# Kernel tuning notes

Measured on AMD Instinct MI355X. Metric: run time of the kernel, lower is better.

Reference implementation:

```python
import jax, jax.numpy as jnp
import numpy as np

EPS = 1e-5  # PyG LayerNorm default eps
N, E, D, H, B = 100000, 1600000, 128, 256, 64


def _gcn_edge_weights(src, dst, n):
    # GCNConv symmetric normalization with added self-loops:
    # deg[i] = in-degree(i) + 1 ; w(j->i) = deg[j]^-1/2 * deg[i]^-1/2
    deg = jax.ops.segment_sum(jnp.ones(src.shape[0], jnp.float32), dst, num_segments=n) + 1.0
    dinv = jax.lax.rsqrt(deg)
    return dinv[src] * dinv[dst], 1.0 / deg  # edge weights, self-loop weights


def _gcn_conv(x, W, b, src, dst, ew, self_w):
    h = x @ W  # [N, H]
    agg = jax.ops.segment_sum(h[src] * ew[:, None], dst, num_segments=x.shape[0])
    return agg + h * self_w[:, None] + b


def _graph_layernorm(x, batch, batch_size, w, b):
    # PyG LayerNorm(mode='graph'): normalize over all nodes & channels of each graph
    n_feat = x.shape[1]
    cnt = jnp.clip(jax.ops.segment_sum(jnp.ones(x.shape[0], jnp.float32), batch,
                                       num_segments=batch_size), 1.0)
    denom = cnt * n_feat  # elements per graph
    mean = jax.ops.segment_sum(x.sum(-1), batch, num_segments=batch_size) / denom
    xc = x - mean[batch][:, None]
    var = jax.ops.segment_sum((xc * xc).sum(-1), batch, num_segments=batch_size) / denom
    out = xc * jax.lax.rsqrt(var + EPS)[batch][:, None]
    return out * w + b


def setup_inputs() -> dict:
    key = jax.random.key(0)
    ks = jax.random.split(key, 16)
    s = 0.05
    inp = {
        'x': jax.random.normal(ks[0], (N, D), jnp.float32),
        'W1': jax.random.normal(ks[1], (D, H), jnp.float32) * s,
        'b1': jnp.zeros((H,), jnp.float32),
        'ln1_w': jnp.ones((H,), jnp.float32), 'ln1_b': jnp.zeros((H,), jnp.float32),
        'W2': jax.random.normal(ks[2], (H, H), jnp.float32) * s,
        'b2': jnp.zeros((H,), jnp.float32),
        'ln2_w': jnp.ones((H,), jnp.float32), 'ln2_b': jnp.zeros((H,), jnp.float32),
        'W3': jax.random.normal(ks[3], (H, H), jnp.float32) * s,
        'b3': jnp.zeros((H,), jnp.float32),
        'ln3_w': jnp.ones((H,), jnp.float32), 'ln3_b': jnp.zeros((H,), jnp.float32),
        'jk_w': jax.random.normal(ks[4], (3 * H, H), jnp.float32) * s,
        'jk_b': jnp.zeros((H,), jnp.float32),
        'fc1_w': jax.random.normal(ks[5], (H, H // 2), jnp.float32) * s,
        'fc1_b': jnp.zeros((H // 2,), jnp.float32),
        'fc2_w': jax.random.normal(ks[6], (H // 2, 1), jnp.float32) * s,
        'fc2_b': jnp.zeros((1,), jnp.float32),
        'edge_index': jax.random.randint(ks[7], (2, E), 0, N, dtype=jnp.int64)
                      if jax.config.jax_enable_x64 else jax.random.randint(ks[7], (2, E), 0, N),
        'batch': jnp.sort(jax.random.randint(ks[8], (N,), 0, B)),
        'batch_size': B,
    }
    return inp


def reference(x, W1, b1, ln1_w, ln1_b, W2, b2, ln2_w, ln2_b, W3, b3, ln3_w, ln3_b,
              jk_w, jk_b, fc1_w, fc1_b, fc2_w, fc2_b, edge_index, batch, batch_size):
    src, dst = edge_index[0], edge_index[1]
    ew, self_w = _gcn_edge_weights(src, dst, x.shape[0])
    xs = []
    h = x
    for (W, b, lw, lb) in ((W1, b1, ln1_w, ln1_b), (W2, b2, ln2_w, ln2_b),
                           (W3, b3, ln3_w, ln3_b)):
        h = _gcn_conv(h, W, b, src, dst, ew, self_w)
        h = _graph_layernorm(h, batch, batch_size, lw, lb)
        h = jnp.tanh(h)  # act_first=False: norm then act; dropout is identity in eval
        xs.append(h)
    h = jnp.concatenate(xs, axis=-1) @ jk_w + jk_b  # JK 'cat' + final lin
    h = jnp.tanh(h @ fc1_w + fc1_b)
    v = h @ fc2_w + fc2_b  # [N, 1]
    # last node index of each (sorted, consecutive) graph id
    last_idx = jnp.searchsorted(batch, jnp.arange(batch_size), side='right') - 1
    return v[last_idx]  # [batch_size, 1]
```

## Files before the change

### kernel.cpp

```cpp
#include <hip/hip_runtime.h>
#include <hip/hip_bf16.h>
#include <hip/hip_fp16.h>
#include <math.h>

#define HDIM 256
#define NGRAPH 64
#define SCAN_CHUNK 2048

__device__ inline __half2 u2h2(unsigned u) { return *reinterpret_cast<__half2*>(&u); }
__device__ inline unsigned h22u(__half2 h) { return *reinterpret_cast<unsigned*>(&h); }

typedef _Float16 f16x8 __attribute__((ext_vector_type(8)));
typedef float    f32x4 __attribute__((ext_vector_type(4)));

__global__ void deg_count_k(const int* __restrict__ dst, int* __restrict__ deg, int E, int n) {
    int i = blockIdx.x * blockDim.x + threadIdx.x;
    if (i < E) {
        int d = dst[i];
        if ((unsigned)d < (unsigned)n) atomicAdd(&deg[d], 1);
    }
}

__global__ void dinv_k(const int* __restrict__ deg, float* __restrict__ dinv, int n) {
    int i = blockIdx.x * blockDim.x + threadIdx.x;
    if (i < n) dinv[i] = 1.0f / sqrtf((float)deg[i] + 1.0f);
}

__global__ void last_idx_k(const int* __restrict__ batch, int* __restrict__ lastidx, int n) {
    int i = blockIdx.x * blockDim.x + threadIdx.x;
    if (i < n) {
        int b = batch[i];
        if ((i == n - 1 || batch[i + 1] != b) && b >= 0 && b < NGRAPH) lastidx[b] = i;
    }
}

__global__ void cvt_x_k(const float* __restrict__ x, __half* __restrict__ xh, long n4) {
    long i = (long)blockIdx.x * blockDim.x + threadIdx.x;
    if (i < n4) {
        float4 v = *(const float4*)(x + i * 4);
        __half2 p0 = __float22half2_rn(make_float2(v.x, v.y));
        __half2 p1 = __float22half2_rn(make_float2(v.z, v.w));
        uint2 st; st.x = h22u(p0); st.y = h22u(p1);
        *(uint2*)(xh + i * 4) = st;
    }
}

__global__ void cvt_w_k(const float* __restrict__ W, __half* __restrict__ Wt, int K) {
    int idx = blockIdx.x * 256 + threadIdx.x;
    int k = idx >> 8, c = idx & 255;
    if (k < K) Wt[(size_t)c * K + k] = __float2half(W[(size_t)k * HDIM + c]);
}

__global__ __launch_bounds__(256) void scan1_k(const int* __restrict__ deg,
                                               int* __restrict__ partial, int n) {
    __shared__ int sm[256];
    int t = threadIdx.x;
    int base = blockIdx.x * SCAN_CHUNK + t * 8;
    int s = 0;
#pragma unroll
    for (int j = 0; j < 8; j++) { int idx = base + j; if (idx < n) s += deg[idx]; }
    sm[t] = s; __syncthreads();
    for (int o = 128; o; o >>= 1) { if (t < o) sm[t] += sm[t + o]; __syncthreads(); }
    if (t == 0) partial[blockIdx.x] = sm[0];
}

__global__ __launch_bounds__(1024) void scan2_k(int* __restrict__ partial, int nb,
                                                int* __restrict__ rs, int n) {
    __shared__ int sm[1024];
    int t = threadIdx.x;
    int v = (t < nb) ? partial[t] : 0;
    sm[t] = v; __syncthreads();
    for (int o = 1; o < 1024; o <<= 1) {
        int add = (t >= o) ? sm[t - o] : 0;
        __syncthreads();
        sm[t] += add;
        __syncthreads();
    }
    if (t < nb) partial[t] = sm[t] - v;
    if (t == nb - 1) rs[n] = sm[t];
}

__global__ __launch_bounds__(256) void scan3_k(const int* __restrict__ deg,
                                               const int* __restrict__ partial,
                                               int* __restrict__ rs, int* __restrict__ cur, int n) {
    __shared__ int sm[256];
    int t = threadIdx.x;
    int base = blockIdx.x * SCAN_CHUNK + t * 8;
    int loc[8]; int s = 0;
#pragma unroll
    for (int j = 0; j < 8; j++) {
        int idx = base + j;
        loc[j] = (idx < n) ? deg[idx] : 0;
        s += loc[j];
    }
    sm[t] = s; __syncthreads();
    int v = s;
    for (int o = 1; o < 256; o <<= 1) {
        int add = (t >= o) ? sm[t - o] : 0;
        __syncthreads();
        sm[t] += add;
        __syncthreads();
    }
    int run = partial[blockIdx.x] + sm[t] - v;
#pragma unroll
    for (int j = 0; j < 8; j++) {
        int idx = base + j;
        if (idx < n) { rs[idx] = run; cur[idx] = run; }
        run += loc[j];
    }
}

__global__ void scatter_k(const int* __restrict__ src, const int* __restrict__ dst,
                          int* __restrict__ cur, int* __restrict__ csr, int E, int n) {
    int e = blockIdx.x * blockDim.x + threadIdx.x;
    if (e < E) {
        int d = dst[e], s = src[e];
        if ((unsigned)d < (unsigned)n && (unsigned)s < (unsigned)n) {
            int pos = atomicAdd(&cur[d], 1);
            csr[pos] = s;
        }
    }
}

template <int DIM>
__global__ __launch_bounds__(256) void agg_csr_k(
    const int* __restrict__ rs, const int* __restrict__ csr,
    const __half* __restrict__ xin, const float* __restrict__ dinv,
    __half* __restrict__ z, int n) {
    constexpr int LPR  = DIM / 8;
    constexpr int NSUB = 64 / LPR;
    int wid  = (blockIdx.x * blockDim.x + threadIdx.x) >> 6;
    int lane = threadIdx.x & 63;
    int nw   = (gridDim.x * blockDim.x) >> 6;
    const int h  = lane / LPR;
    const int sl = lane % LPR;

    for (int i = wid; i < n; i += nw) {
        int j0 = rs[i], j1 = rs[i + 1];
        float acc[8];
#pragma unroll
        for (int v = 0; v < 8; v++) acc[v] = 0.0f;

        for (int jb = j0; jb < j1; jb += 64) {
            int m = j1 - jb; if (m > 64) m = 64;
            int   sj = (lane < m) ? csr[jb + lane] : 0;
            float wj = (lane < m) ? dinv[sj] : 0.0f;
#pragma unroll 4
            for (int r = 0; r < m; r += NSUB) {
                int   s = __shfl(sj, r + h);
                float w = __shfl(wj, r + h);
                const __half* xr = xin + (size_t)s * DIM + sl * 8;
                uint4 u = *(const uint4*)xr;
                float2 a0 = __half22float2(u2h2(u.x));
                float2 a1 = __half22float2(u2h2(u.y));
                float2 a2 = __half22float2(u2h2(u.z));
                float2 a3 = __half22float2(u2h2(u.w));
                acc[0] += a0.x * w; acc[1] += a0.y * w;
                acc[2] += a1.x * w; acc[3] += a1.y * w;
                acc[4] += a2.x * w; acc[5] += a2.y * w;
                acc[6] += a3.x * w; acc[7] += a3.y * w;
            }
        }

        if (NSUB == 4) {
#pragma unroll
            for (int v = 0; v < 8; v++) acc[v] += __shfl_xor(acc[v], 16);
        }
#pragma unroll
        for (int v = 0; v < 8; v++) acc[v] += __shfl_xor(acc[v], 32);

        if (h == 0) {
            float di  = dinv[i];
            float di2 = di * di;
            const __half* xr = xin + (size_t)i * DIM + sl * 8;
            uint4 u = *(const uint4*)xr;
            float2 a0 = __half22float2(u2h2(u.x));
            float2 a1 = __half22float2(u2h2(u.y));
            float2 a2 = __half22float2(u2h2(u.z));
            float2 a3 = __half22float2(u2h2(u.w));
            float o0 = di * acc[0] + di2 * a0.x, o1 = di * acc[1] + di2 * a0.y;
            float o2 = di * acc[2] + di2 * a1.x, o3 = di * acc[3] + di2 * a1.y;
            float o4 = di * acc[4] + di2 * a2.x, o5 = di * acc[5] + di2 * a2.y;
            float o6 = di * acc[6] + di2 * a3.x, o7 = di * acc[7] + di2 * a3.y;
            uint4 st;
            st.x = h22u(__float22half2_rn(make_float2(o0, o1)));
            st.y = h22u(__float22half2_rn(make_float2(o2, o3)));
            st.z = h22u(__float22half2_rn(make_float2(o4, o5)));
            st.w = h22u(__float22half2_rn(make_float2(o6, o7)));
            *(uint4*)(z + (size_t)i * DIM + sl * 8) = st;
        }
    }
}

template <int K>
__global__ __launch_bounds__(256) void gcn_gemm_k(
    const __half* __restrict__ z, const __half* __restrict__ Wt,
    const float* __restrict__ bias, float* __restrict__ hout, int n) {
    const int t   = threadIdx.x;
    const int wv  = t >> 6;
    const int l   = t & 63;
    const int l15 = l & 15;
    const int lhi = l >> 4;
    const int r0  = blockIdx.x * 32;
    const int c0  = wv * 64;

    f32x4 acc[2][4];
#pragma unroll
    for (int cg = 0; cg < 4; cg++) {
        float bv = bias[c0 + cg * 16 + l15];
        f32x4 b4 = {bv, bv, bv, bv};
        acc[0][cg] = b4;
        acc[1][cg] = b4;
    }

    int ra = r0 + l15;      if (ra >= n) ra = n - 1;
    int rb = r0 + 16 + l15; if (rb >= n) rb = n - 1;
    const __half* za = z + (size_t)ra * K + lhi * 8;
    const __half* zb = z + (size_t)rb * K + lhi * 8;
    const __half* wp0 = Wt + (size_t)(c0 + 0 * 16 + l15) * K + lhi * 8;
    const __half* wp1 = Wt + (size_t)(c0 + 1 * 16 + l15) * K + lhi * 8;
    const __half* wp2 = Wt + (size_t)(c0 + 2 * 16 + l15) * K + lhi * 8;
    const __half* wp3 = Wt + (size_t)(c0 + 3 * 16 + l15) * K + lhi * 8;

#pragma unroll
    for (int ks = 0; ks < K; ks += 32) {
        f16x8 a0 = *(const f16x8*)(za + ks);
        f16x8 a1 = *(const f16x8*)(zb + ks);
        f16x8 b0 = *(const f16x8*)(wp0 + ks);
        f16x8 b1 = *(const f16x8*)(wp1 + ks);
        f16x8 b2 = *(const f16x8*)(wp2 + ks);
        f16x8 b3 = *(const f16x8*)(wp3 + ks);
        acc[0][0] = __builtin_amdgcn_mfma_f32_16x16x32_f16(a0, b0, acc[0][0], 0, 0, 0);
        acc[1][0] = __builtin_amdgcn_mfma_f32_16x16x32_f16(a1, b0, acc[1][0], 0, 0, 0);
        acc[0][1] = __builtin_amdgcn_mfma_f32_16x16x32_f16(a0, b1, acc[0][1], 0, 0, 0);
        acc[1][1] = __builtin_amdgcn_mfma_f32_16x16x32_f16(a1, b1, acc[1][1], 0, 0, 0);
        acc[0][2] = __builtin_amdgcn_mfma_f32_16x16x32_f16(a0, b2, acc[0][2], 0, 0, 0);
        acc[1][2] = __builtin_amdgcn_mfma_f32_16x16x32_f16(a1, b2, acc[1][2], 0, 0, 0);
        acc[0][3] = __builtin_amdgcn_mfma_f32_16x16x32_f16(a0, b3, acc[0][3], 0, 0, 0);
        acc[1][3] = __builtin_amdgcn_mfma_f32_16x16x32_f16(a1, b3, acc[1][3], 0, 0, 0);
    }

#pragma unroll
    for (int rg = 0; rg < 2; rg++) {
#pragma unroll
        for (int i = 0; i < 4; i++) {
            int r = r0 + rg * 16 + lhi * 4 + i;
            if (r < n) {
                float* hp = hout + (size_t)r * HDIM + c0 + l15;
#pragma unroll
                for (int cg = 0; cg < 4; cg++)
                    hp[cg * 16] = acc[rg][cg][i];
            }
        }
    }
}

__global__ __launch_bounds__(256) void ln_stats_k(
    const float* __restrict__ h, const int* __restrict__ batch,
    float* __restrict__ gsum, float* __restrict__ gsq, int n, int npb) {
    __shared__ float lsum[NGRAPH], lsq[NGRAPH];
    int t = threadIdx.x;
    if (t < NGRAPH) { lsum[t] = 0.0f; lsq[t] = 0.0f; }
    __syncthreads();
    int wv = t >> 6, lane = t & 63;
    int i0 = blockIdx.x * npb;
    int i1 = i0 + npb; if (i1 > n) i1 = n;
    for (int i = i0 + wv; i < i1; i += 4) {
        float4 v = *(const float4*)(h + (size_t)i * HDIM + lane * 4);
        float s = v.x + v.y + v.z + v.w;
        float q = v.x * v.x + v.y * v.y + v.z * v.z + v.w * v.w;
        for (int o = 32; o; o >>= 1) {
            s += __shfl_down(s, o);
            q += __shfl_down(q, o);
        }
        if (lane == 0) {
            int b = batch[i];
            if (b < 0) b = 0; if (b >= NGRAPH) b = NGRAPH - 1;
            atomicAdd(&lsum[b], s);
            atomicAdd(&lsq[b], q);
        }
    }
    __syncthreads();
    if (t < NGRAPH) {
        float s = lsum[t], q = lsq[t];
        if (s != 0.0f || q != 0.0f) {
            unsafeAtomicAdd(&gsum[t], s);
            unsafeAtomicAdd(&gsq[t], q);
        }
    }
}

__global__ void ln_fin_k(const float* __restrict__ gsum, const float* __restrict__ gsq,
                         const int* __restrict__ lastidx, float* __restrict__ mean,
                         float* __restrict__ rstd, int n) {
    int g = threadIdx.x;
    if (g >= NGRAPH) return;
    int last = lastidx[g];
    if (last < 0) last = 0; if (last >= n) last = n - 1;
    int prev = g ? lastidx[g - 1] : -1;
    if (prev < -1) prev = -1; if (prev >= n) prev = n - 1;
    float cnt = (float)(last - prev);
    if (cnt < 1.0f) cnt = 1.0f;
    float denom = cnt * (float)HDIM;
    float m = gsum[g] / denom;
    float v = gsq[g] / denom - m * m;
    if (v < 0.0f) v = 0.0f;
    mean[g] = m;
    rstd[g] = 1.0f / sqrtf(v + 1e-5f);
}

__global__ void ln_tanh_k(const float* __restrict__ h, const int* __restrict__ batch,
                          const float* __restrict__ mean, const float* __restrict__ rstd,
                          const float* __restrict__ w, const float* __restrict__ b,
                          __half* __restrict__ h16, int n) {
    long gid = (long)blockIdx.x * blockDim.x + threadIdx.x;
    long total = (long)n * 64;
    if (gid >= total) return;
    int i  = (int)(gid >> 6);
    int c  = (int)(gid & 63) * 4;
    int bg = batch[i];
    if (bg < 0) bg = 0; if (bg >= NGRAPH) bg = NGRAPH - 1;
    float m = mean[bg], r = rstd[bg];
    float4 v  = *(const float4*)(h + (size_t)i * HDIM + c);
    float4 w4 = *(const float4*)(w + c);
    float4 b4 = *(const float4*)(b + c);
    v.x = tanhf((v.x - m) * r * w4.x + b4.x);
    v.y = tanhf((v.y - m) * r * w4.y + b4.y);
    v.z = tanhf((v.z - m) * r * w4.z + b4.z);
    v.w = tanhf((v.w - m) * r * w4.w + b4.w);
    __half2 p0 = __float22half2_rn(make_float2(v.x, v.y));
    __half2 p1 = __float22half2_rn(make_float2(v.z, v.w));
    uint2 st; st.x = h22u(p0); st.y = h22u(p1);
    *(uint2*)(h16 + (size_t)i * HDIM + c) = st;
}

__global__ void extract_rows_k(const __half* __restrict__ x, const int* __restrict__ lastidx,
                               float* __restrict__ out, int n) {
    int g = blockIdx.x, c = threadIdx.x;
    int r = lastidx[g];
    if (r < 0) r = 0; if (r >= n) r = n - 1;
    out[(size_t)g * HDIM + c] = __half2float(x[(size_t)r * HDIM + c]);
}

__global__ __launch_bounds__(256) void final_mlp_k(
    const float* __restrict__ xjk,
    const float* __restrict__ jk_w, const float* __restrict__ jk_b,
    const float* __restrict__ fc1_w, const float* __restrict__ fc1_b,
    const float* __restrict__ fc2_w, const float* __restrict__ fc2_b,
    float* __restrict__ out) {
    __shared__ float vec[3 * HDIM];
    __shared__ float h1[HDIM];
    __shared__ float h2[128];
    int g = blockIdx.x, t = threadIdx.x;
    vec[t]            = xjk[(size_t)0 * NGRAPH * HDIM + (size_t)g * HDIM + t];
    vec[HDIM + t]     = xjk[(size_t)1 * NGRAPH * HDIM + (size_t)g * HDIM + t];
    vec[2 * HDIM + t] = xjk[(size_t)2 * NGRAPH * HDIM + (size_t)g * HDIM + t];
    __syncthreads();
    float a = jk_b[t];
    for (int k = 0; k < 3 * HDIM; k++) a += vec[k] * jk_w[(size_t)k * HDIM + t];
    h1[t] = a;
    __syncthreads();
    if (t < 128) {
        float a2 = fc1_b[t];
        for (int k = 0; k < HDIM; k++) a2 += h1[k] * fc1_w[(size_t)k * 128 + t];
        h2[t] = tanhf(a2);
    }
    __syncthreads();
    if (t < 64) {
        float a3 = h2[t] * fc2_w[t] + h2[t + 64] * fc2_w[t + 64];
        for (int o = 32; o; o >>= 1) a3 += __shfl_down(a3, o);
        if (t == 0) out[g] = a3 + fc2_b[0];
    }
}

extern "C" void kernel_launch(void* const* d_in, const int* in_sizes, int n_in,
                              void* d_out, int out_size, void* d_ws, size_t ws_size,
                              hipStream_t stream) {
    const float* x    = (const float*)d_in[0];
    const float* W1   = (const float*)d_in[1];
    const float* b1   = (const float*)d_in[2];
    const float* ln1w = (const float*)d_in[3];
    const float* ln1b = (const float*)d_in[4];
    const float* W2   = (const float*)d_in[5];
    const float* b2   = (const float*)d_in[6];
    const float* ln2w = (const float*)d_in[7];
    const float* ln2b = (const float*)d_in[8];
    const float* W3   = (const float*)d_in[9];
    const float* b3   = (const float*)d_in[10];
    const float* ln3w = (const float*)d_in[11];
    const float* ln3b = (const float*)d_in[12];
    const float* jkw  = (const float*)d_in[13];
    const float* jkb  = (const float*)d_in[14];
    const float* fc1w = (const float*)d_in[15];
    const float* fc1b = (const float*)d_in[16];
    const float* fc2w = (const float*)d_in[17];
    const float* fc2b = (const float*)d_in[18];
    const int*  eidx  = (const int*)d_in[19];
    const int*  batch = (const int*)d_in[20];

    const int E = in_sizes[19] / 2;
    const int n = in_sizes[20];
    const int D = in_sizes[0] / n;

    const int* src = eidx;
    const int* dst = eidx + E;

    char* base = (char*)d_ws;
    size_t o = 0;
    auto alloc = [&](size_t bytes) { void* p = base + o; o += (bytes + 255) & ~(size_t)255; return p; };
    __half* bufZ = (__half*)alloc((size_t)n * HDIM * 2);
    float*  bufH = (float*)alloc((size_t)n * HDIM * 4);
    __half* hF   = (__half*)alloc((size_t)n * HDIM * 2);
    __half* Wt   = (__half*)alloc((size_t)HDIM * HDIM * 2);
    int*   csr  = (int*)alloc((size_t)E * 4);
    int*   rs   = (int*)alloc((size_t)(n + 1) * 4);
    int*   cur  = (int*)alloc((size_t)n * 4);
    int*   degi = (int*)alloc((size_t)n * 4);
    float* dinv = (float*)alloc((size_t)n * 4);
    int*   part = (int*)alloc(1024 * 4);
    float* xjk  = (float*)alloc((size_t)3 * NGRAPH * HDIM * 4);
    int*   lidx = (int*)alloc(NGRAPH * 4);
    float* gsum = (float*)alloc(NGRAPH * 4);
    float* gsq  = (float*)alloc(NGRAPH * 4);
    float* mean = (float*)alloc(NGRAPH * 4);
    float* rstd = (float*)alloc(NGRAPH * 4);
    (void)ws_size;

    float* out = (float*)d_out;
    const int GB = (n + 31) / 32;
    const int NB = (n + SCAN_CHUNK - 1) / SCAN_CHUNK;
    const int AB = 2048;
    const int SB = 1024;
    const int NPB = (n + SB - 1) / SB;

    hipMemsetAsync(degi, 0, (size_t)n * 4, stream);
    hipMemsetAsync(lidx, 0, NGRAPH * 4, stream);
    deg_count_k<<<(E + 255) / 256, 256, 0, stream>>>(dst, degi, E, n);
    dinv_k<<<(n + 255) / 256, 256, 0, stream>>>(degi, dinv, n);
    last_idx_k<<<(n + 255) / 256, 256, 0, stream>>>(batch, lidx, n);
    scan1_k<<<NB, 256, 0, stream>>>(degi, part, n);
    scan2_k<<<1, 1024, 0, stream>>>(part, NB, rs, n);
    scan3_k<<<NB, 256, 0, stream>>>(degi, part, rs, cur, n);
    scatter_k<<<(E + 255) / 256, 256, 0, stream>>>(src, dst, cur, csr, E, n);
    long n4 = (long)n * D / 4;
    cvt_x_k<<<(int)((n4 + 255) / 256), 256, 0, stream>>>(x, hF, n4);

    agg_csr_k<128><<<AB, 256, 0, stream>>>(rs, csr, hF, dinv, bufZ, n);
    cvt_w_k<<<128, 256, 0, stream>>>(W1, Wt, 128);
    gcn_gemm_k<128><<<GB, 256, 0, stream>>>(bufZ, Wt, b1, bufH, n);
    hipMemsetAsync(gsum, 0, 2 * NGRAPH * 4, stream);
    ln_stats_k<<<SB, 256, 0, stream>>>(bufH, batch, gsum, gsq, n, NPB);
    ln_fin_k<<<1, 64, 0, stream>>>(gsum, gsq, lidx, mean, rstd, n);
    ln_tanh_k<<<(int)(((long)n * 64 + 255) / 256), 256, 0, stream>>>(bufH, batch, mean, rstd, ln1w, ln1b, hF, n);
    extract_rows_k<<<NGRAPH, 256, 0, stream>>>(hF, lidx, xjk + 0 * NGRAPH * HDIM, n);

    agg_csr_k<256><<<AB, 256, 0, stream>>>(rs, csr, hF, dinv, bufZ, n);
    cvt_w_k<<<256, 256, 0, stream>>>(W2, Wt, 256);
    gcn_gemm_k<256><<<GB, 256, 0, stream>>>(bufZ, Wt, b2, bufH, n);
    hipMemsetAsync(gsum, 0, 2 * NGRAPH * 4, stream);
    ln_stats_k<<<SB, 256, 0, stream>>>(bufH, batch, gsum, gsq, n, NPB);
    ln_fin_k<<<1, 64, 0, stream>>>(gsum, gsq, lidx, mean, rstd, n);
    ln_tanh_k<<<(int)(((long)n * 64 + 255) / 256), 256, 0, stream>>>(bufH, batch, mean, rstd, ln2w, ln2b, hF, n);
    extract_rows_k<<<NGRAPH, 256, 0, stream>>>(hF, lidx, xjk + 1 * NGRAPH * HDIM, n);

    agg_csr_k<256><<<AB, 256, 0, stream>>>(rs, csr, hF, dinv, bufZ, n);
    cvt_w_k<<<256, 256, 0, stream>>>(W3, Wt, 256);
    gcn_gemm_k<256><<<GB, 256, 0, stream>>>(bufZ, Wt, b3, bufH, n);
    hipMemsetAsync(gsum, 0, 2 * NGRAPH * 4, stream);
    ln_stats_k<<<SB, 256, 0, stream>>>(bufH, batch, gsum, gsq, n, NPB);
    ln_fin_k<<<1, 64, 0, stream>>>(gsum, gsq, lidx, mean, rstd, n);
    ln_tanh_k<<<(int)(((long)n * 64 + 255) / 256), 256, 0, stream>>>(bufH, batch, mean, rstd, ln3w, ln3b, hF, n);
    extract_rows_k<<<NGRAPH, 256, 0, stream>>>(hF, lidx, xjk + 2 * NGRAPH * HDIM, n);

    final_mlp_k<<<NGRAPH, 256, 0, stream>>>(xjk, jkw, jkb, fc1w, fc1b, fc2w, fc2b, out);
}
```

Measured before the change: 1.079 ms.

## Fuse LayerNorm statistics into GEMM epilogue and store pre-norm activations as fp16

The GEMM epilogue now accumulates per-row sums and squared sums in shared memory, reduces them per graph, and atomically adds them to the global stats. This removes the separate ln_stats pass over the activation buffer. The pre-norm activations are also written as fp16 instead of fp32, which halves the write traffic and the read traffic in ln_tanh. The costs are shared-memory atomics and two extra barriers in the GEMM, scalar 2-byte strided stores, and lower precision of the stored pre-norm values.

```diff
diff --git a/kernel.cpp b/kernel.cpp
--- a/kernel.cpp
+++ b/kernel.cpp
@@ -195,7 +195,11 @@
 template <int K>
 __global__ __launch_bounds__(256) void gcn_gemm_k(
     const __half* __restrict__ z, const __half* __restrict__ Wt,
-    const float* __restrict__ bias, float* __restrict__ hout, int n) {
+    const float* __restrict__ bias, __half* __restrict__ hout,
+    const int* __restrict__ batch, float* __restrict__ gsum,
+    float* __restrict__ gsq, int n) {
+    __shared__ float rowsum[32], rowsq[32];
+    __shared__ float lgs[NGRAPH], lgq[NGRAPH];
     const int t   = threadIdx.x;
     const int wv  = t >> 6;
     const int l   = t & 63;
@@ -203,6 +207,9 @@
     const int lhi = l >> 4;
     const int r0  = blockIdx.x * 32;
     const int c0  = wv * 64;
+
+    if (t < 32) { rowsum[t] = 0.0f; rowsq[t] = 0.0f; }
+    if (t < NGRAPH) { lgs[t] = 0.0f; lgq[t] = 0.0f; }
 
     f32x4 acc[2][4];
 #pragma unroll
@@ -240,49 +247,41 @@
         acc[1][3] = __builtin_amdgcn_mfma_f32_16x16x32_f16(a1, b3, acc[1][3], 0, 0, 0);
     }
 
+    __syncthreads();
+
 #pragma unroll
     for (int rg = 0; rg < 2; rg++) {
 #pragma unroll
         for (int i = 0; i < 4; i++) {
-            int r = r0 + rg * 16 + lhi * 4 + i;
+            int ri = rg * 16 + lhi * 4 + i;
+            int r  = r0 + ri;
             if (r < n) {
-                float* hp = hout + (size_t)r * HDIM + c0 + l15;
-#pragma unroll
-                for (int cg = 0; cg < 4; cg++)
-                    hp[cg * 16] = acc[rg][cg][i];
+                __half* hp = hout + (size_t)r * HDIM + c0 + l15;
+                float v0 = acc[rg][0][i], v1 = acc[rg][1][i];
+                float v2 = acc[rg][2][i], v3 = acc[rg][3][i];
+                hp[0]  = __float2half(v0);
+                hp[16] = __float2half(v1);
+                hp[32] = __float2half(v2);
+                hp[48] = __float2half(v3);
+                atomicAdd(&rowsum[ri], v0 + v1 + v2 + v3);
+                atomicAdd(&rowsq[ri], v0 * v0 + v1 * v1 + v2 * v2 + v3 * v3);
             }
         }
     }
-}
-
-__global__ __launch_bounds__(256) void ln_stats_k(
-    const float* __restrict__ h, const int* __restrict__ batch,
-    float* __restrict__ gsum, float* __restrict__ gsq, int n, int npb) {
-    __shared__ float lsum[NGRAPH], lsq[NGRAPH];
-    int t = threadIdx.x;
-    if (t < NGRAPH) { lsum[t] = 0.0f; lsq[t] = 0.0f; }
-    __syncthreads();
-    int wv = t >> 6, lane = t & 63;
-    int i0 = blockIdx.x * npb;
-    int i1 = i0 + npb; if (i1 > n) i1 = n;
-    for (int i = i0 + wv; i < i1; i += 4) {
-        float4 v = *(const float4*)(h + (size_t)i * HDIM + lane * 4);
-        float s = v.x + v.y + v.z + v.w;
-        float q = v.x * v.x + v.y * v.y + v.z * v.z + v.w * v.w;
-        for (int o = 32; o; o >>= 1) {
-            s += __shfl_down(s, o);
-            q += __shfl_down(q, o);
-        }
-        if (lane == 0) {
-            int b = batch[i];
-            if (b < 0) b = 0; if (b >= NGRAPH) b = NGRAPH - 1;
-            atomicAdd(&lsum[b], s);
-            atomicAdd(&lsq[b], q);
+    __syncthreads();
+
+    if (t < 32) {
+        int r = r0 + t;
+        if (r < n) {
+            int bg = batch[r];
+            if (bg < 0) bg = 0; if (bg >= NGRAPH) bg = NGRAPH - 1;
+            atomicAdd(&lgs[bg], rowsum[t]);
+            atomicAdd(&lgq[bg], rowsq[t]);
         }
     }
     __syncthreads();
     if (t < NGRAPH) {
-        float s = lsum[t], q = lsq[t];
+        float s = lgs[t], q = lgq[t];
         if (s != 0.0f || q != 0.0f) {
             unsafeAtomicAdd(&gsum[t], s);
             unsafeAtomicAdd(&gsq[t], q);
@@ -309,7 +308,7 @@
     rstd[g] = 1.0f / sqrtf(v + 1e-5f);
 }
 
-__global__ void ln_tanh_k(const float* __restrict__ h, const int* __restrict__ batch,
+__global__ void ln_tanh_k(const __half* __restrict__ h, const int* __restrict__ batch,
                           const float* __restrict__ mean, const float* __restrict__ rstd,
                           const float* __restrict__ w, const float* __restrict__ b,
                           __half* __restrict__ h16, int n) {
@@ -321,16 +320,18 @@
     int bg = batch[i];
     if (bg < 0) bg = 0; if (bg >= NGRAPH) bg = NGRAPH - 1;
     float m = mean[bg], r = rstd[bg];
-    float4 v  = *(const float4*)(h + (size_t)i * HDIM + c);
+    uint2 u = *(const uint2*)(h + (size_t)i * HDIM + c);
+    float2 a0 = __half22float2(u2h2(u.x));
+    float2 a1 = __half22float2(u2h2(u.y));
     float4 w4 = *(const float4*)(w + c);
     float4 b4 = *(const float4*)(b + c);
-    v.x = tanhf((v.x - m) * r * w4.x + b4.x);
-    v.y = tanhf((v.y - m) * r * w4.y + b4.y);
-    v.z = tanhf((v.z - m) * r * w4.z + b4.z);
-    v.w = tanhf((v.w - m) * r * w4.w + b4.w);
-    __half2 p0 = __float22half2_rn(make_float2(v.x, v.y));
-    __half2 p1 = __float22half2_rn(make_float2(v.z, v.w));
-    uint2 st; st.x = h22u(p0); st.y = h22u(p1);
+    float v0 = tanhf((a0.x - m) * r * w4.x + b4.x);
+    float v1 = tanhf((a0.y - m) * r * w4.y + b4.y);
+    float v2 = tanhf((a1.x - m) * r * w4.z + b4.z);
+    float v3 = tanhf((a1.y - m) * r * w4.w + b4.w);
+    uint2 st;
+    st.x = h22u(__float22half2_rn(make_float2(v0, v1)));
+    st.y = h22u(__float22half2_rn(make_float2(v2, v3)));
     *(uint2*)(h16 + (size_t)i * HDIM + c) = st;
 }
 
@@ -409,7 +410,7 @@
     size_t o = 0;
     auto alloc = [&](size_t bytes) { void* p = base + o; o += (bytes + 255) & ~(size_t)255; return p; };
     __half* bufZ = (__half*)alloc((size_t)n * HDIM * 2);
-    float*  bufH = (float*)alloc((size_t)n * HDIM * 4);
+    __half* hPre = (__half*)alloc((size_t)n * HDIM * 2);
     __half* hF   = (__half*)alloc((size_t)n * HDIM * 2);
     __half* Wt   = (__half*)alloc((size_t)HDIM * HDIM * 2);
     int*   csr  = (int*)alloc((size_t)E * 4);
@@ -430,8 +431,7 @@
     const int GB = (n + 31) / 32;
     const int NB = (n + SCAN_CHUNK - 1) / SCAN_CHUNK;
     const int AB = 2048;
-    const int SB = 1024;
-    const int NPB = (n + SB - 1) / SB;
+    const int LT = (int)(((long)n * 64 + 255) / 256);
 
     hipMemsetAsync(degi, 0, (size_t)n * 4, stream);
     hipMemsetAsync(lidx, 0, NGRAPH * 4, stream);
@@ -447,29 +447,26 @@
 
     agg_csr_k<128><<<AB, 256, 0, stream>>>(rs, csr, hF, dinv, bufZ, n);
     cvt_w_k<<<128, 256, 0, stream>>>(W1, Wt, 128);
-    gcn_gemm_k<128><<<GB, 256, 0, stream>>>(bufZ, Wt, b1, bufH, n);
     hipMemsetAsync(gsum, 0, 2 * NGRAPH * 4, stream);
-    ln_stats_k<<<SB, 256, 0, stream>>>(bufH, batch, gsum, gsq, n, NPB);
+    gcn_gemm_k<128><<<GB, 256, 0, stream>>>(bufZ, Wt, b1, hPre, batch, gsum, gsq, n);
     ln_fin_k<<<1, 64, 0, stream>>>(gsum, gsq, lidx, mean, rstd, n);
-    ln_tanh_k<<<(int)(((long)n * 64 + 255) / 256), 256, 0, stream>>>(bufH, batch, mean, rstd, ln1w, ln1b, hF, n);
+    ln_tanh_k<<<LT, 256, 0, stream>>>(hPre, batch, mean, rstd, ln1w, ln1b, hF, n);
     extract_rows_k<<<NGRAPH, 256, 0, stream>>>(hF, lidx, xjk + 0 * NGRAPH * HDIM, n);
 
     agg_csr_k<256><<<AB, 256, 0, stream>>>(rs, csr, hF, dinv, bufZ, n);
     cvt_w_k<<<256, 256, 0, stream>>>(W2, Wt, 256);
-    gcn_gemm_k<256><<<GB, 256, 0, stream>>>(bufZ, Wt, b2, bufH, n);
     hipMemsetAsync(gsum, 0, 2 * NGRAPH * 4, stream);
-    ln_stats_k<<<SB, 256, 0, stream>>>(bufH, batch, gsum, gsq, n, NPB);
+    gcn_gemm_k<256><<<GB, 256, 0, stream>>>(bufZ, Wt, b2, hPre, batch, gsum, gsq, n);
     ln_fin_k<<<1, 64, 0, stream>>>(gsum, gsq, lidx, mean, rstd, n);
-    ln_tanh_k<<<(int)(((long)n * 64 + 255) / 256), 256, 0, stream>>>(bufH, batch, mean, rstd, ln2w, ln2b, hF, n);
+    ln_tanh_k<<<LT, 256, 0, stream>>>(hPre, batch, mean, rstd, ln2w, ln2b, hF, n);
     extract_rows_k<<<NGRAPH, 256, 0, stream>>>(hF, lidx, xjk + 1 * NGRAPH * HDIM, n);
 
     agg_csr_k<256><<<AB, 256, 0, stream>>>(rs, csr, hF, dinv, bufZ, n);
     cvt_w_k<<<256, 256, 0, stream>>>(W3, Wt, 256);
-    gcn_gemm_k<256><<<GB, 256, 0, stream>>>(bufZ, Wt, b3, bufH, n);
     hipMemsetAsync(gsum, 0, 2 * NGRAPH * 4, stream);
-    ln_stats_k<<<SB, 256, 0, stream>>>(bufH, batch, gsum, gsq, n, NPB);
+    gcn_gemm_k<256><<<GB, 256, 0, stream>>>(bufZ, Wt, b3, hPre, batch, gsum, gsq, n);
     ln_fin_k<<<1, 64, 0, stream>>>(gsum, gsq, lidx, mean, rstd, n);
-    ln_tanh_k<<<(int)(((long)n * 64 + 255) / 256), 256, 0, stream>>>(bufH, batch, mean, rstd, ln3w, ln3b, hF, n);
+    ln_tanh_k<<<LT, 256, 0, stream>>>(hPre, batch, mean, rstd, ln3w, ln3b, hF, n);
     extract_rows_k<<<NGRAPH, 256, 0, stream>>>(hF, lidx, xjk + 2 * NGRAPH * HDIM, n);
 
     final_mlp_k<<<NGRAPH, 256, 0, stream>>>(xjk, jkw, jkb, fc1w, fc1b, fc2w, fc2b, out);
```

New measurement: 1.200 ms. +11.2%, slower.
